# Kernel optimization log

Hardware: AMD Instinct MI355X
Metric: run time of the kernel (lower is better)

## Reference

```python
import jax, jax.numpy as jnp
import numpy as np

B, K, N = 8192, 10, 100
LAM = 1.0


def _vec_transpose_P():
    # 9x9 vec-transpose permutation: P[3i+j, 3j+i] = 1 (the _getP matrix)
    P = np.zeros((9, 9), dtype=np.float32)
    for i in range(3):
        for j in range(3):
            P[3 * i + j, 3 * j + i] = 1.0
    return jnp.asarray(P)


def setup_inputs() -> dict:
    key = jax.random.key(0)
    k1, k2, k3 = jax.random.split(key, 3)
    weights = jax.random.uniform(k1, (N, 1), dtype=jnp.float32) + 0.1  # positive weights
    model_keypoints = jax.random.normal(k2, (K, 3, N), dtype=jnp.float32)
    y = jax.random.normal(k3, (B, 3, N), dtype=jnp.float32)
    return {"y": y, "weights": weights, "model_keypoints": model_keypoints}


def _pace_forward(y, weights, model_keypoints):
    n = model_keypoints.shape[-1]
    k = model_keypoints.shape[0]
    bsz = y.shape[0]
    w = weights                                  # (N,1)
    wsum = w.sum()
    b = model_keypoints                          # (K,3,N)
    b_w = (b @ w) / wsum                         # (K,3,1)
    sw = jnp.sqrt(w[:, 0])                       # (N,)

    # ---- precomputed constants (original __init__) ----
    bar_b = sw[None, None, :] * (b - b_w)                    # (K,3,N)
    bar_B = bar_b.transpose(0, 2, 1).reshape(k, 3 * n).T     # (3N,K), row idx 3n+a
    bar_H = 2.0 * (bar_B.T @ bar_B + LAM * jnp.eye(k, dtype=y.dtype))
    Hinv = jnp.linalg.inv(bar_H)
    Ht = Hinv @ jnp.ones((k, 1), dtype=y.dtype)
    denom = Ht.sum()
    G = Hinv - (Ht @ Ht.T) / denom               # (K,K)
    g = Ht / denom                               # (K,1)
    GBt = G @ bar_B.T                            # (K,3N)
    M = jnp.concatenate([2.0 * bar_B @ GBt - jnp.eye(3 * n, dtype=y.dtype),
                         2.0 * jnp.sqrt(LAM) * GBt], axis=0)       # (3N+K,3N)
    h = jnp.concatenate([bar_B @ g, jnp.sqrt(LAM) * g], axis=0)    # (3N+K,1)
    P = _vec_transpose_P().astype(y.dtype)

    # ---- forward ----
    y_w = (y @ w) / wsum                         # (B,3,1)
    bar_y = sw[None, None, :] * (y - y_w)        # (B,3,N)

    # E_b = M @ kron(Ybar_b^T, I3) @ P, done batched without materializing kron:
    # (M @ kron(Y^T, I3))[m, 3j+a] = sum_n M[m, 3n+a] * Y[j, n]
    Mr = M.reshape(-1, n, 3)                                  # Mr[m, nn, a] = M[m, 3nn+a]
    MB = jnp.einsum('mna,bjn->bmja', Mr, bar_y)               # (B,3N+K,3,3)
    E = MB.reshape(bsz, -1, 9) @ P                            # (B,3N+K,9)
    q00 = h[:, 0] @ h[:, 0]                                   # scalar h^T h
    hE = jnp.einsum('m,bmc->bc', h[:, 0], E)                  # (B,9)
    Q11 = jnp.einsum('bmc,bmd->bcd', E, E)                    # (B,9,9)
    top = jnp.concatenate([jnp.broadcast_to(q00, (bsz, 1, 1)), hE[:, None, :]], axis=2)
    bot = jnp.concatenate([hE[:, :, None], Q11], axis=2)
    Q = jnp.concatenate([top, bot], axis=1)                   # (B,10,10)

    # SDP relaxation: at a tight optimum X = v v^T with v the minimizer of v^T Q v,
    # recovered here as the eigenvector of Q with smallest eigenvalue (batched eigh)
    _, evec = jnp.linalg.eigh(Q)
    v = evec[:, :, 0]                                         # (B,10), ascending order
    v = v / v[:, :1]                                          # homogenize: v[0] = 1
    R = v[:, 1:].reshape(bsz, 3, 3).transpose(0, 2, 1)        # (B,3,3)

    # shape coefficients: c = 2 * G B^T * kron(I_N, R^T) vec(bar_y) + g
    RTy = jnp.einsum('bra,brn->bna', R, bar_y).reshape(bsz, 3 * n)   # idx 3n+a
    c = 2.0 * jnp.einsum('km,bm->bk', GBt, RTy)[:, :, None] + g[None, :, :]  # (B,K,1)
    # translation: t = y_w - R b_w^T c
    t = y_w - R @ jnp.einsum('ka,bko->bao', b_w[:, :, 0], c)  # (B,3,1)
    return R, t, c


def reference(y, weights, model_keypoints):
    return _pace_forward(y, weights, model_keypoints)
```

## Files before the change

kernel.cpp:

```cpp
#include <hip/hip_runtime.h>
#include <math.h>

#define SM_WSUM 0
#define SM_RWS  1
#define SM_Q00  2
#define SM_Z2   4
#define SM_BS   16
#define SM_W    48
#define SM_G    148
#define SM_GV   248
#define SM_BW   260
#define SM_SIZE 292

__host__ __device__ constexpr int TRI(int p, int q) { return p*10 - (p*(p+1))/2 + q; }
__host__ __device__ constexpr int SIDX(int a, int b) { return (a<=b) ? TRI(a,b) : TRI(b,a); }

__global__ __launch_bounds__(64, 1) void pace_fused(const float* __restrict__ y,
                                                    const float* __restrict__ w,
                                                    const float* __restrict__ mk,
                                                    float* __restrict__ out) {
  __shared__ __attribute__((aligned(16))) float sc[3200];
  __shared__ float sm[SM_SIZE];
  __shared__ __attribute__((aligned(16))) float scr[5760];
  const int tid = threadIdx.x;
  const int b = blockIdx.x*64 + tid;
  const float* yb = y + b*300;

  float4 c0 = *(const float4*)(yb);
  float4 c1 = *(const float4*)(yb+100);
  float4 c2 = *(const float4*)(yb+200);

  float yw[3];

  {
    float* s_mb = scr;
    float* s_w  = scr+3000;
    float* s_sw = scr+3104;
    float* s_bw = scr+3208;
    float* s_C  = scr+3240;
    float* s_Hi = scr+3340;
    float* s_G  = scr+3440;
    float* s_T  = scr+3540;
    float* s_gv = scr+3640;
    float* s_Ht = scr+3656;
    float* s_z  = scr+3672;

    for (int i=tid;i<3000;i+=64) s_mb[i]=mk[i];
    for (int i=tid;i<100;i+=64){ float x=w[i]; s_w[i]=x; s_sw[i]=sqrtf(x); }
    __syncthreads();

    float a = s_w[tid] + ((tid<36)? s_w[tid+64] : 0.f);
    #pragma unroll
    for (int m=32;m;m>>=1) a += __shfl_xor(a,m);
    const float wsum = a;
    const float rws = 1.0f/a;

    if (tid<30){
      const float4* p=(const float4*)&s_mb[tid*100];
      const float4* q=(const float4*)&s_w[0];
      float acc=0;
      #pragma unroll 5
      for (int j=0;j<25;j++){ float4 x=p[j], yv=q[j];
        acc=fmaf(x.x,yv.x,acc); acc=fmaf(x.y,yv.y,acc);
        acc=fmaf(x.z,yv.z,acc); acc=fmaf(x.w,yv.w,acc); }
      s_bw[tid]=acc*rws;
    }
    __syncthreads();
    for (int i=tid;i<3000;i+=64){ int r=i/100, n=i-r*100; s_mb[i]=s_sw[n]*(s_mb[i]-s_bw[r]); }
    __syncthreads();
    for (int e=tid;e<100;e+=64){
      int k=e/10, k2=e-10*k;
      const float4* p1=(const float4*)&s_mb[k*300];
      const float4* p2=(const float4*)&s_mb[k2*300];
      float acc=0;
      #pragma unroll 5
      for (int j=0;j<75;j++){ float4 x=p1[j], yv=p2[j];
        acc=fmaf(x.x,yv.x,acc); acc=fmaf(x.y,yv.y,acc);
        acc=fmaf(x.z,yv.z,acc); acc=fmaf(x.w,yv.w,acc); }
      s_C[e]=acc;
    }
    __syncthreads();
    float R[20];
    {
      int row=(tid<10)? tid : 0;
      #pragma unroll
      for (int c=0;c<10;c++) R[c]=2.0f*(s_C[row*10+c]+(c==row?1.0f:0.0f));
      #pragma unroll
      for (int c=0;c<10;c++) R[10+c]=(c==row)?1.0f:0.0f;
    }
    #pragma unroll
    for (int p=0;p<10;p++){
      float appv=__shfl(R[p],p);
      float ra=1.0f/appv;
      float fr=R[p];
      #pragma unroll
      for (int c=0;c<20;c++){
        float pc=__shfl(R[c],p)*ra;
        R[c]=(tid==p)? pc : fmaf(-fr,pc,R[c]);
      }
    }
    float ht=0.f;
    if (tid<10){
      #pragma unroll
      for (int c=0;c<10;c++){ s_Hi[tid*10+c]=R[10+c]; ht+=R[10+c]; }
      s_Ht[tid]=ht;
    }
    float hv=(tid<10)? ht : 0.f;
    #pragma unroll
    for (int m=32;m;m>>=1) hv+=__shfl_xor(hv,m);
    const float rden=1.0f/hv;
    if (tid<10) s_gv[tid]=ht*rden;
    __syncthreads();
    for (int e=tid;e<100;e+=64){ int r=e/10,c=e-10*r; s_G[e]=s_Hi[e]-s_Ht[r]*s_Ht[c]*rden; }
    __syncthreads();
    for (int e=tid;e<100;e+=64){
      int r=e/10,c=e-10*r; float acc=0;
      #pragma unroll
      for (int j=0;j<10;j++) acc+=(s_C[r*10+j]+(r==j?1.0f:0.0f))*s_G[j*10+c];
      s_T[e]=acc;
    }
    __syncthreads();
    for (int e=tid;e<100;e+=64){
      int r=e/10,c=e-10*r; float acc=0;
      #pragma unroll
      for (int j=0;j<10;j++) acc+=s_G[r*10+j]*s_T[j*10+c];
      sm[SM_W+e]=4.0f*acc-4.0f*s_G[e];
      sm[SM_G+e]=s_G[e];
    }
    if (tid<10){
      float acc=0;
      #pragma unroll
      for (int j=0;j<10;j++) acc+=(s_C[tid*10+j]+(tid==j?1.0f:0.0f))*s_gv[j];
      s_z[tid]=acc;
    }
    __syncthreads();
    if (tid<10){
      float acc=0;
      #pragma unroll
      for (int j=0;j<10;j++) acc+=s_G[tid*10+j]*s_z[j];
      sm[SM_Z2+tid]=2.0f*acc-s_gv[tid];
    }
    float qv=0.f;
    if (tid<10){
      float acc=0;
      #pragma unroll
      for (int c=0;c<10;c++) acc+=s_C[tid*10+c]*s_gv[c];
      qv=s_gv[tid]*acc+s_gv[tid]*s_gv[tid];
    }
    #pragma unroll
    for (int m=32;m;m>>=1) qv+=__shfl_xor(qv,m);
    if (tid==0){ sm[SM_WSUM]=wsum; sm[SM_RWS]=rws; sm[SM_Q00]=qv; sm[3]=0.f; }
    for (int i=tid;i<3200;i+=64){
      int n=i>>5, e=i&31; float v;
      if (e==0) v=s_w[n];
      else if (e==31) v=0.f;
      else v=s_mb[(e-1)*100+n]*s_sw[n];
      sc[i]=v;
    }
    if (tid<30){
      const float4* p=(const float4*)&s_mb[tid*100];
      const float4* q=(const float4*)&s_sw[0];
      float acc=0;
      #pragma unroll 5
      for (int j=0;j<25;j++){ float4 x=p[j], yv=q[j];
        acc=fmaf(x.x,yv.x,acc); acc=fmaf(x.y,yv.y,acc);
        acc=fmaf(x.z,yv.z,acc); acc=fmaf(x.w,yv.w,acc); }
      sm[SM_BS+tid]=acc;
    }
    if (tid<10) sm[SM_GV+tid]=s_gv[tid];
    if (tid<30) sm[SM_BW+tid]=s_bw[tid];
    __syncthreads();
  }

  float* sF = scr;

  float swy0=0,swy1=0,swy2=0;
  float s00=0,s01=0,s02=0,s11=0,s12=0,s22=0;
  float F0[90];
  #pragma unroll
  for (int i=0;i<90;i++) F0[i]=0.f;

  #pragma unroll 1
  for (int g=0; g<25; ++g) {
    float4 n0, n1, n2;
    if (g<24) {
      n0 = *(const float4*)(yb+4*g+4);
      n1 = *(const float4*)(yb+104+4*g);
      n2 = *(const float4*)(yb+204+4*g);
    }
    float ax[4]={c0.x,c0.y,c0.z,c0.w};
    float bx[4]={c1.x,c1.y,c1.z,c1.w};
    float gx[4]={c2.x,c2.y,c2.z,c2.w};
    #pragma unroll
    for (int u=0;u<4;u++) {
      const int n = 4*g+u;
      float cf[32];
      const float4* cp = (const float4*)&sc[n*32];
      #pragma unroll
      for (int r=0;r<8;r++) ((float4*)cf)[r] = cp[r];
      float y0=ax[u], y1=bx[u], y2=gx[u];
      float wn=cf[0];
      float wy0=wn*y0, wy1=wn*y1, wy2=wn*y2;
      swy0+=wy0; swy1+=wy1; swy2+=wy2;
      s00+=wy0*y0; s01+=wy0*y1; s02+=wy0*y2; s11+=wy1*y1; s12+=wy1*y2; s22+=wy2*y2;
      #pragma unroll
      for (int k=0;k<10;k++) {
        #pragma unroll
        for (int j=0;j<3;j++) {
          float bcv=cf[1+k*3+j];
          F0[k*9+j*3+0]+=bcv*y0; F0[k*9+j*3+1]+=bcv*y1; F0[k*9+j*3+2]+=bcv*y2;
        }
      }
    }
    if (g<24) { c0=n0; c1=n1; c2=n2; }
  }

  const float wsum=sm[SM_WSUM], rws=sm[SM_RWS], q00=sm[SM_Q00];
  yw[0]=swy0*rws; yw[1]=swy1*rws; yw[2]=swy2*rws;
  float G3[9];
  G3[0]=s00-wsum*yw[0]*yw[0];
  G3[4]=s11-wsum*yw[1]*yw[1];
  G3[8]=s22-wsum*yw[2]*yw[2];
  G3[1]=G3[3]=s01-wsum*yw[0]*yw[1];
  G3[2]=G3[6]=s02-wsum*yw[0]*yw[2];
  G3[5]=G3[7]=s12-wsum*yw[1]*yw[2];
  #pragma unroll
  for (int k=0;k<10;k++)
    #pragma unroll
    for (int j=0;j<3;j++)
      #pragma unroll
      for (int i=0;i<3;i++)
        F0[k*9+j*3+i] -= yw[i]*sm[SM_BS+k*3+j];
  #pragma unroll
  for (int m=0;m<90;m++) sF[m*64+tid]=F0[m];
  float hE[9];
  #pragma unroll
  for (int m=0;m<9;m++) {
    float acc=0;
    #pragma unroll
    for (int k=0;k<10;k++) acc += sm[SM_Z2+k]*F0[k*9+m];
    hE[m]=acc;
  }

  float A[55];
  A[TRI(0,0)]=q00;
  #pragma unroll
  for (int m=0;m<9;m++) A[TRI(0,1+m)]=hE[m];
  #pragma unroll
  for (int mp=0;mp<9;mp++) {
    float t2[10];
    #pragma unroll
    for (int k=0;k<10;k++) {
      float acc=0;
      #pragma unroll
      for (int k2=0;k2<10;k2++) acc += sm[SM_W+k*10+k2]*F0[k2*9+mp];
      t2[k]=acc;
    }
    #pragma unroll
    for (int m=0;m<9;m++) {
      if (m>mp) continue;
      float acc = ((m/3)==(mp/3)) ? G3[(m%3)*3+(mp%3)] : 0.f;
      #pragma unroll
      for (int k=0;k<10;k++) acc += F0[k*9+m]*t2[k];
      A[TRI(1+m,1+mp)]=acc;
    }
  }

  constexpr int OFFK[8] = {0,9,17,24,30,35,39,42};
  float vhh[44], beta[8], ee[9];

  #pragma unroll
  for (int k=0;k<8;k++) {
    float nrm2 = 0.f;
    #pragma unroll
    for (int i=1;i<10;i++){ if (i<k+1) continue; float xi=A[SIDX(i,k)]; nrm2=fmaf(xi,xi,nrm2); }
    float x0 = A[SIDX(k+1,k)];
    float nr = sqrtf(nrm2);
    float alpha = -copysignf(nr, x0);
    bool ok = nrm2 > 1e-30f;
    float v1 = x0 - alpha;
    float vtv = -2.0f*alpha*v1;
    float bh = ok ? 2.0f*__builtin_amdgcn_rcpf(vtv) : 0.f;
    beta[k]=bh; ee[k]= ok ? alpha : x0;
    float vv[10];
    #pragma unroll
    for (int i=0;i<10;i++){
      if (i<k+1) { vv[i]=0.f; continue; }
      vv[i] = (i==k+1)? v1 : A[SIDX(i,k)];
    }
    #pragma unroll
    for (int i=0;i<9;i++){ if (i>=9-k) break; vhh[OFFK[k]+i]=vv[k+1+i]; }
    float p[10];
    #pragma unroll
    for (int i=0;i<10;i++){
      if (i<k+1){ p[i]=0.f; continue; }
      float acc=0;
      #pragma unroll
      for (int j=1;j<10;j++){ if (j<k+1) continue; acc += A[SIDX(i,j)]*vv[j]; }
      p[i]=bh*acc;
    }
    float Kc=0.f;
    #pragma unroll
    for (int i=1;i<10;i++){ if (i<k+1) continue; Kc = fmaf(vv[i],p[i],Kc); }
    Kc *= 0.5f*bh;
    float wv[10];
    #pragma unroll
    for (int i=0;i<10;i++){ wv[i] = p[i] - Kc*vv[i]; }
    #pragma unroll
    for (int i=1;i<10;i++){
      if (i<k+1) continue;
      #pragma unroll
      for (int j=1;j<10;j++){
        if (j<i) continue;
        A[TRI(i,j)] -= vv[i]*wv[j] + wv[i]*vv[j];
      }
    }
  }
  ee[8] = A[TRI(8,9)];
  float dd[10];
  #pragma unroll
  for (int i=0;i<10;i++) dd[i]=A[TRI(i,i)];
  float esq[9];
  #pragma unroll
  for (int i=0;i<9;i++) esq[i]=ee[i]*ee[i];

  float scaleT=0.f, lo=1e30f, hi=1e30f;
  #pragma unroll
  for (int i=0;i<10;i++){
    float r = ((i>0)?fabsf(ee[i-1]):0.f) + ((i<9)?fabsf(ee[i]):0.f);
    scaleT = fmaxf(scaleT, fabsf(dd[i])+r);
    lo = fminf(lo, dd[i]-r);
    hi = fminf(hi, dd[i]);
  }
  hi += 1e-6f*scaleT + 1e-30f;
  const float pm = 1e-12f*scaleT + 1e-37f;

  #pragma unroll 1
  for (int it=0; it<18; ++it){
    float mid = 0.5f*(lo+hi);
    float q = dd[0]-mid;
    q = (fabsf(q)<pm) ? ((q<0.f)?-pm:pm) : q;
    int cnt = (q<0.f);
    #pragma unroll
    for (int i=1;i<10;i++){
      q = dd[i]-mid - esq[i-1]*__builtin_amdgcn_rcpf(q);
      q = (fabsf(q)<pm) ? ((q<0.f)?-pm:pm) : q;
      cnt += (q<0.f);
    }
    bool any = cnt>0;
    hi = any? mid : hi;
    lo = any? lo : mid;
  }
  const float sigma = lo - 1e-5f*scaleT - 1e-30f;
  const float pmL = 1e-8f*scaleT + 1e-37f;

  float lfac[9], iq[10];
  {
    float q = fmaxf(dd[0]-sigma, pmL);
    iq[0]=__builtin_amdgcn_rcpf(q);
    #pragma unroll
    for (int i=1;i<10;i++){
      lfac[i-1] = ee[i-1]*iq[i-1];
      q = fmaxf(dd[i]-sigma - ee[i-1]*lfac[i-1], pmL);
      iq[i]=__builtin_amdgcn_rcpf(q);
    }
  }
  float xv[10];
  #pragma unroll
  for (int i=0;i<10;i++) xv[i]=1.f;
  #pragma unroll 1
  for (int itr=0; itr<3; ++itr){
    #pragma unroll
    for (int i=1;i<10;i++){ float v = xv[i] - lfac[i-1]*xv[i-1]; xv[i]=fminf(fmaxf(v,-1e15f),1e15f); }
    #pragma unroll
    for (int i=0;i<10;i++){ float v = xv[i]*iq[i]; xv[i]=fminf(fmaxf(v,-1e15f),1e15f); }
    #pragma unroll
    for (int i=8;i>=0;i--){ float v = xv[i] - lfac[i]*xv[i+1]; xv[i]=fminf(fmaxf(v,-1e15f),1e15f); }
    float nn=0.f;
    #pragma unroll
    for (int i=0;i<10;i++) nn = fmaf(xv[i],xv[i],nn);
    nn = fmaxf(nn, 1e-30f);
    float sc2 = rsqrtf(nn);
    #pragma unroll
    for (int i=0;i<10;i++) xv[i]*=sc2;
  }
  #pragma unroll
  for (int k=7;k>=0;k--){
    float s=0.f;
    #pragma unroll
    for (int i=0;i<9;i++){ if (i>=9-k) break; s = fmaf(vhh[OFFK[k]+i], xv[k+1+i], s); }
    s *= beta[k];
    #pragma unroll
    for (int i=0;i<9;i++){ if (i>=9-k) break; xv[k+1+i] -= s*vhh[OFFK[k]+i]; }
  }

  float r0 = 1.0f/xv[0];
  float vn[10];
  vn[0]=1.f;
  #pragma unroll
  for (int m=1;m<10;m++) vn[m]=xv[m]*r0;

  #pragma unroll
  for (int i=0;i<3;i++)
    #pragma unroll
    for (int j=0;j<3;j++)
      out[b*9 + i*3 + j] = vn[1+3*j+i];

  float d[10];
  #pragma unroll
  for (int k=0;k<10;k++) {
    float acc=0;
    #pragma unroll
    for (int m=0;m<9;m++) acc += vn[1+m]*sF[(k*9+m)*64+tid];
    d[k]=acc;
  }
  float cv[10];
  #pragma unroll
  for (int k=0;k<10;k++) {
    float acc=0;
    #pragma unroll
    for (int k2=0;k2<10;k2++) acc += sm[SM_G+k*10+k2]*d[k2];
    cv[k]=2.0f*acc + sm[SM_GV+k];
  }
  float e0=0,e1=0,e2v=0;
  #pragma unroll
  for (int k=0;k<10;k++) {
    e0 += sm[SM_BW+k*3+0]*cv[k];
    e1 += sm[SM_BW+k*3+1]*cv[k];
    e2v += sm[SM_BW+k*3+2]*cv[k];
  }
  #pragma unroll
  for (int i=0;i<3;i++) {
    float tv = yw[i] - (vn[1+0+i]*e0 + vn[1+3+i]*e1 + vn[1+6+i]*e2v);
    out[8192*9 + b*3 + i] = tv;
  }
  #pragma unroll
  for (int k=0;k<10;k++)
    out[8192*12 + b*10 + k] = cv[k];
}

extern "C" void kernel_launch(void* const* d_in, const int* in_sizes, int n_in,
                              void* d_out, int out_size, void* d_ws, size_t ws_size,
                              hipStream_t stream) {
  const float* y  = (const float*)d_in[0];
  const float* w  = (const float*)d_in[1];
  const float* mk = (const float*)d_in[2];
  float* out = (float*)d_out;
  pace_fused<<<128, 64, 0, stream>>>(y, w, mk, out);
}
```

Before: 120.3 us.

## Split each batch item across 8 lanes with DPP reductions and parallel bisection

Each batch item is now handled by 8 cooperating lanes instead of one, which raises the grid from 128 to 1024 blocks. The lanes split the N-loop accumulation and combine partial sums with DPP reductions, build Q columns in parallel through shared memory, and run a 9-way multisection eigenvalue search using ballot. The inverse iteration now works on a Cholesky factor of the shifted original Q, so the Householder back-transformation is dropped. The aim is to fill far more of the GPU than 128 single-wave blocks could. The cost is redundant per-block setup (the K×K inverse and constants are recomputed in all 1024 blocks), extra syncthreads, and fewer bisection steps, which may change precision.

```diff
diff --git a/kernel.cpp b/kernel.cpp
--- a/kernel.cpp
+++ b/kernel.cpp
@@ -12,25 +12,34 @@
 #define SM_BW   260
 #define SM_SIZE 292
 
-__host__ __device__ constexpr int TRI(int p, int q) { return p*10 - (p*(p+1))/2 + q; }
-__host__ __device__ constexpr int SIDX(int a, int b) { return (a<=b) ? TRI(a,b) : TRI(b,a); }
-
-__global__ __launch_bounds__(64, 1) void pace_fused(const float* __restrict__ y,
-                                                    const float* __restrict__ w,
-                                                    const float* __restrict__ mk,
-                                                    float* __restrict__ out) {
-  __shared__ __attribute__((aligned(16))) float sc[3200];
+__host__ __device__ constexpr int TRI(int p,int q){ return p*10-(p*(p+1))/2+q; }
+__host__ __device__ constexpr int SIDX(int a,int b){ return (a<=b)?TRI(a,b):TRI(b,a); }
+__host__ __device__ constexpr int LTRI(int i,int j){ return i*(i+1)/2+j; }
+
+template<int CTRL>
+__device__ __forceinline__ float dpp_add(float v){
+  int s = __builtin_amdgcn_mov_dpp(__float_as_int(v), CTRL, 0xF, 0xF, true);
+  return v + __int_as_float(s);
+}
+__device__ __forceinline__ float gsum8(float v){
+  v = dpp_add<0xB1>(v);
+  v = dpp_add<0x4E>(v);
+  v = dpp_add<0x141>(v);
+  return v;
+}
+
+__global__ __launch_bounds__(64,1) void pace_fused(const float* __restrict__ y,
+                                                   const float* __restrict__ w,
+                                                   const float* __restrict__ mk,
+                                                   float* __restrict__ out){
+  __shared__ __attribute__((aligned(16))) float sc[3600];
   __shared__ float sm[SM_SIZE];
-  __shared__ __attribute__((aligned(16))) float scr[5760];
-  const int tid = threadIdx.x;
-  const int b = blockIdx.x*64 + tid;
-  const float* yb = y + b*300;
-
-  float4 c0 = *(const float4*)(yb);
-  float4 c1 = *(const float4*)(yb+100);
-  float4 c2 = *(const float4*)(yb+200);
-
-  float yw[3];
+  __shared__ __attribute__((aligned(16))) float scr[3712];
+  const int tid  = threadIdx.x;
+  const int sub  = tid & 7;
+  const int item = tid >> 3;
+  const int gb   = blockIdx.x*8 + item;
+  const float* yb = y + gb*300;
 
   {
     float* s_mb = scr;
@@ -150,10 +159,10 @@
     #pragma unroll
     for (int m=32;m;m>>=1) qv+=__shfl_xor(qv,m);
     if (tid==0){ sm[SM_WSUM]=wsum; sm[SM_RWS]=rws; sm[SM_Q00]=qv; sm[3]=0.f; }
-    for (int i=tid;i<3200;i+=64){
-      int n=i>>5, e=i&31; float v;
+    for (int i=tid;i<3600;i+=64){
+      int n=i/36, e=i-36*n; float v;
       if (e==0) v=s_w[n];
-      else if (e==31) v=0.f;
+      else if (e>=31) v=0.f;
       else v=s_mb[(e-1)*100+n]*s_sw[n];
       sc[i]=v;
     }
@@ -172,152 +181,179 @@
     __syncthreads();
   }
 
-  float* sF = scr;
-
-  float swy0=0,swy1=0,swy2=0;
-  float s00=0,s01=0,s02=0,s11=0,s12=0,s22=0;
+  float* sF  = scr;
+  float* sD  = scr+736;
+  float* sQl = scr+832;
+  float* sG3 = scr+1280;
+
   float F0[90];
   #pragma unroll
   for (int i=0;i<90;i++) F0[i]=0.f;
-
-  #pragma unroll 1
-  for (int g=0; g<25; ++g) {
-    float4 n0, n1, n2;
-    if (g<24) {
-      n0 = *(const float4*)(yb+4*g+4);
-      n1 = *(const float4*)(yb+104+4*g);
-      n2 = *(const float4*)(yb+204+4*g);
-    }
-    float ax[4]={c0.x,c0.y,c0.z,c0.w};
-    float bx[4]={c1.x,c1.y,c1.z,c1.w};
-    float gx[4]={c2.x,c2.y,c2.z,c2.w};
-    #pragma unroll
-    for (int u=0;u<4;u++) {
-      const int n = 4*g+u;
-      float cf[32];
-      const float4* cp = (const float4*)&sc[n*32];
-      #pragma unroll
-      for (int r=0;r<8;r++) ((float4*)cf)[r] = cp[r];
-      float y0=ax[u], y1=bx[u], y2=gx[u];
-      float wn=cf[0];
-      float wy0=wn*y0, wy1=wn*y1, wy2=wn*y2;
-      swy0+=wy0; swy1+=wy1; swy2+=wy2;
-      s00+=wy0*y0; s01+=wy0*y1; s02+=wy0*y2; s11+=wy1*y1; s12+=wy1*y2; s22+=wy2*y2;
-      #pragma unroll
-      for (int k=0;k<10;k++) {
+  float swy0=0,swy1=0,swy2=0,s00=0,s01=0,s02=0,s11=0,s12=0,s22=0;
+
+  #pragma unroll
+  for (int mrep=0;mrep<4;++mrep){
+    int g=sub+8*mrep;
+    if (g<25){
+      float4 a4=*(const float4*)(yb+4*g);
+      float4 b4=*(const float4*)(yb+100+4*g);
+      float4 g4=*(const float4*)(yb+200+4*g);
+      float ax[4]={a4.x,a4.y,a4.z,a4.w};
+      float bx[4]={b4.x,b4.y,b4.z,b4.w};
+      float gx[4]={g4.x,g4.y,g4.z,g4.w};
+      #pragma unroll
+      for (int u=0;u<4;u++){
+        const float* cf=&sc[(4*g+u)*36];
+        float c[32];
         #pragma unroll
-        for (int j=0;j<3;j++) {
-          float bcv=cf[1+k*3+j];
-          F0[k*9+j*3+0]+=bcv*y0; F0[k*9+j*3+1]+=bcv*y1; F0[k*9+j*3+2]+=bcv*y2;
+        for (int r=0;r<8;r++) ((float4*)c)[r]=((const float4*)cf)[r];
+        float y0=ax[u],y1=bx[u],y2=gx[u];
+        float wn=c[0];
+        float wy0=wn*y0,wy1=wn*y1,wy2=wn*y2;
+        swy0+=wy0;swy1+=wy1;swy2+=wy2;
+        s00+=wy0*y0;s01+=wy0*y1;s02+=wy0*y2;s11+=wy1*y1;s12+=wy1*y2;s22+=wy2*y2;
+        #pragma unroll
+        for (int k=0;k<10;k++){
+          #pragma unroll
+          for (int j=0;j<3;j++){
+            float bcv=c[1+k*3+j];
+            F0[k*9+j*3+0]+=bcv*y0;
+            F0[k*9+j*3+1]+=bcv*y1;
+            F0[k*9+j*3+2]+=bcv*y2;
+          }
         }
       }
     }
-    if (g<24) { c0=n0; c1=n1; c2=n2; }
-  }
-
-  const float wsum=sm[SM_WSUM], rws=sm[SM_RWS], q00=sm[SM_Q00];
-  yw[0]=swy0*rws; yw[1]=swy1*rws; yw[2]=swy2*rws;
-  float G3[9];
-  G3[0]=s00-wsum*yw[0]*yw[0];
-  G3[4]=s11-wsum*yw[1]*yw[1];
-  G3[8]=s22-wsum*yw[2]*yw[2];
-  G3[1]=G3[3]=s01-wsum*yw[0]*yw[1];
-  G3[2]=G3[6]=s02-wsum*yw[0]*yw[2];
-  G3[5]=G3[7]=s12-wsum*yw[1]*yw[2];
-  #pragma unroll
-  for (int k=0;k<10;k++)
-    #pragma unroll
-    for (int j=0;j<3;j++)
-      #pragma unroll
-      for (int i=0;i<3;i++)
-        F0[k*9+j*3+i] -= yw[i]*sm[SM_BS+k*3+j];
-  #pragma unroll
-  for (int m=0;m<90;m++) sF[m*64+tid]=F0[m];
-  float hE[9];
-  #pragma unroll
-  for (int m=0;m<9;m++) {
-    float acc=0;
-    #pragma unroll
-    for (int k=0;k<10;k++) acc += sm[SM_Z2+k]*F0[k*9+m];
-    hE[m]=acc;
-  }
+  }
+  #pragma unroll
+  for (int e=0;e<90;e++) F0[e]=gsum8(F0[e]);
+  swy0=gsum8(swy0); swy1=gsum8(swy1); swy2=gsum8(swy2);
+  s00=gsum8(s00); s01=gsum8(s01); s02=gsum8(s02);
+  s11=gsum8(s11); s12=gsum8(s12); s22=gsum8(s22);
+
+  const float wsum=sm[SM_WSUM], rws=sm[SM_RWS];
+  const float yw0=swy0*rws, yw1=swy1*rws, yw2=swy2*rws;
+  float G3r[9];
+  G3r[0]=s00-wsum*yw0*yw0; G3r[4]=s11-wsum*yw1*yw1; G3r[8]=s22-wsum*yw2*yw2;
+  G3r[1]=G3r[3]=s01-wsum*yw0*yw1;
+  G3r[2]=G3r[6]=s02-wsum*yw0*yw2;
+  G3r[5]=G3r[7]=s12-wsum*yw1*yw2;
+  #pragma unroll
+  for (int k=0;k<10;k++){
+    float bs0=sm[SM_BS+k*3+0],bs1=sm[SM_BS+k*3+1],bs2=sm[SM_BS+k*3+2];
+    F0[k*9+0]-=yw0*bs0; F0[k*9+1]-=yw1*bs0; F0[k*9+2]-=yw2*bs0;
+    F0[k*9+3]-=yw0*bs1; F0[k*9+4]-=yw1*bs1; F0[k*9+5]-=yw2*bs1;
+    F0[k*9+6]-=yw0*bs2; F0[k*9+7]-=yw1*bs2; F0[k*9+8]-=yw2*bs2;
+  }
+  if (sub==0){
+    #pragma unroll
+    for (int e=0;e<90;e++) sF[item*90+e]=F0[e];
+    #pragma unroll
+    for (int e=0;e<9;e++) sG3[item*9+e]=G3r[e];
+  }
+  __syncthreads();
+
+  {
+    int mp=sub;
+    float fcol[10], t2[10];
+    #pragma unroll
+    for (int k=0;k<10;k++) fcol[k]=sF[item*90+k*9+mp];
+    #pragma unroll
+    for (int k=0;k<10;k++){
+      float acc=0;
+      #pragma unroll
+      for (int k2=0;k2<10;k2++) acc+=sm[SM_W+k*10+k2]*fcol[k2];
+      t2[k]=acc;
+    }
+    float he=0;
+    #pragma unroll
+    for (int k=0;k<10;k++) he+=sm[SM_Z2+k]*fcol[k];
+    sQl[item*56 + 1+mp]=he;
+    #pragma unroll 1
+    for (int m=0;m<=mp;m++){
+      float gd=sG3[item*9+(m%3)*3+(mp%3)];
+      float acc=((m/3)==(mp/3))? gd : 0.f;
+      #pragma unroll
+      for (int k=0;k<10;k++) acc+=sF[item*90+k*9+m]*t2[k];
+      int p=1+m, q=1+mp;
+      sQl[item*56 + p*10-((p*(p+1))>>1)+q]=acc;
+    }
+    if (sub==0){
+      mp=8;
+      #pragma unroll
+      for (int k=0;k<10;k++) fcol[k]=sF[item*90+k*9+mp];
+      #pragma unroll
+      for (int k=0;k<10;k++){
+        float acc=0;
+        #pragma unroll
+        for (int k2=0;k2<10;k2++) acc+=sm[SM_W+k*10+k2]*fcol[k2];
+        t2[k]=acc;
+      }
+      he=0;
+      #pragma unroll
+      for (int k=0;k<10;k++) he+=sm[SM_Z2+k]*fcol[k];
+      sQl[item*56 + 9]=he;
+      #pragma unroll 1
+      for (int m=0;m<=8;m++){
+        float gd=sG3[item*9+(m%3)*3+2];
+        float acc=((m/3)==2)? gd : 0.f;
+        #pragma unroll
+        for (int k=0;k<10;k++) acc+=sF[item*90+k*9+m]*t2[k];
+        int p=1+m, q=9;
+        sQl[item*56 + p*10-((p*(p+1))>>1)+q]=acc;
+      }
+      sQl[item*56 + 0]=sm[SM_Q00];
+    }
+  }
+  __syncthreads();
 
   float A[55];
-  A[TRI(0,0)]=q00;
-  #pragma unroll
-  for (int m=0;m<9;m++) A[TRI(0,1+m)]=hE[m];
-  #pragma unroll
-  for (int mp=0;mp<9;mp++) {
-    float t2[10];
-    #pragma unroll
-    for (int k=0;k<10;k++) {
-      float acc=0;
-      #pragma unroll
-      for (int k2=0;k2<10;k2++) acc += sm[SM_W+k*10+k2]*F0[k2*9+mp];
-      t2[k]=acc;
-    }
-    #pragma unroll
-    for (int m=0;m<9;m++) {
-      if (m>mp) continue;
-      float acc = ((m/3)==(mp/3)) ? G3[(m%3)*3+(mp%3)] : 0.f;
-      #pragma unroll
-      for (int k=0;k<10;k++) acc += F0[k*9+m]*t2[k];
-      A[TRI(1+m,1+mp)]=acc;
-    }
-  }
-
-  constexpr int OFFK[8] = {0,9,17,24,30,35,39,42};
-  float vhh[44], beta[8], ee[9];
-
-  #pragma unroll
-  for (int k=0;k<8;k++) {
-    float nrm2 = 0.f;
+  #pragma unroll
+  for (int e=0;e<55;e++) A[e]=sQl[item*56+e];
+  float dd[10], ee[9];
+  #pragma unroll
+  for (int k=0;k<8;k++){
+    float nrm2=0.f;
     #pragma unroll
     for (int i=1;i<10;i++){ if (i<k+1) continue; float xi=A[SIDX(i,k)]; nrm2=fmaf(xi,xi,nrm2); }
-    float x0 = A[SIDX(k+1,k)];
-    float nr = sqrtf(nrm2);
-    float alpha = -copysignf(nr, x0);
-    bool ok = nrm2 > 1e-30f;
-    float v1 = x0 - alpha;
-    float vtv = -2.0f*alpha*v1;
-    float bh = ok ? 2.0f*__builtin_amdgcn_rcpf(vtv) : 0.f;
-    beta[k]=bh; ee[k]= ok ? alpha : x0;
+    float x0=A[SIDX(k+1,k)];
+    float nr=sqrtf(nrm2);
+    float alpha=-copysignf(nr,x0);
+    bool ok=nrm2>1e-30f;
+    float v1=x0-alpha;
+    float vtv=-2.0f*alpha*v1;
+    float bh=ok?2.0f*__builtin_amdgcn_rcpf(vtv):0.f;
+    ee[k]=ok?alpha:x0;
     float vv[10];
     #pragma unroll
-    for (int i=0;i<10;i++){
-      if (i<k+1) { vv[i]=0.f; continue; }
-      vv[i] = (i==k+1)? v1 : A[SIDX(i,k)];
-    }
-    #pragma unroll
-    for (int i=0;i<9;i++){ if (i>=9-k) break; vhh[OFFK[k]+i]=vv[k+1+i]; }
+    for (int i=0;i<10;i++) vv[i]=(i<k+1)?0.f:((i==k+1)?v1:A[SIDX(i,k)]);
     float p[10];
     #pragma unroll
     for (int i=0;i<10;i++){
       if (i<k+1){ p[i]=0.f; continue; }
       float acc=0;
       #pragma unroll
-      for (int j=1;j<10;j++){ if (j<k+1) continue; acc += A[SIDX(i,j)]*vv[j]; }
+      for (int j=1;j<10;j++){ if (j<k+1) continue; acc+=A[SIDX(i,j)]*vv[j]; }
       p[i]=bh*acc;
     }
     float Kc=0.f;
     #pragma unroll
-    for (int i=1;i<10;i++){ if (i<k+1) continue; Kc = fmaf(vv[i],p[i],Kc); }
-    Kc *= 0.5f*bh;
+    for (int i=1;i<10;i++){ if (i<k+1) continue; Kc=fmaf(vv[i],p[i],Kc); }
+    Kc*=0.5f*bh;
     float wv[10];
     #pragma unroll
-    for (int i=0;i<10;i++){ wv[i] = p[i] - Kc*vv[i]; }
+    for (int i=0;i<10;i++) wv[i]=p[i]-Kc*vv[i];
     #pragma unroll
     for (int i=1;i<10;i++){
       if (i<k+1) continue;
       #pragma unroll
       for (int j=1;j<10;j++){
         if (j<i) continue;
-        A[TRI(i,j)] -= vv[i]*wv[j] + wv[i]*vv[j];
+        A[TRI(i,j)]-=vv[i]*wv[j]+wv[i]*vv[j];
       }
     }
   }
-  ee[8] = A[TRI(8,9)];
-  float dd[10];
+  ee[8]=A[TRI(8,9)];
   #pragma unroll
   for (int i=0;i<10;i++) dd[i]=A[TRI(i,i)];
   float esq[9];
@@ -327,116 +363,145 @@
   float scaleT=0.f, lo=1e30f, hi=1e30f;
   #pragma unroll
   for (int i=0;i<10;i++){
-    float r = ((i>0)?fabsf(ee[i-1]):0.f) + ((i<9)?fabsf(ee[i]):0.f);
-    scaleT = fmaxf(scaleT, fabsf(dd[i])+r);
-    lo = fminf(lo, dd[i]-r);
-    hi = fminf(hi, dd[i]);
-  }
-  hi += 1e-6f*scaleT + 1e-30f;
-  const float pm = 1e-12f*scaleT + 1e-37f;
-
+    float r=((i>0)?fabsf(ee[i-1]):0.f)+((i<9)?fabsf(ee[i]):0.f);
+    scaleT=fmaxf(scaleT,fabsf(dd[i])+r);
+    lo=fminf(lo,dd[i]-r);
+    hi=fminf(hi,dd[i]);
+  }
+  hi+=1e-6f*scaleT+1e-30f;
+  const float pm=1e-12f*scaleT+1e-37f;
+  const float r9=1.0f/9.0f;
   #pragma unroll 1
-  for (int it=0; it<18; ++it){
-    float mid = 0.5f*(lo+hi);
-    float q = dd[0]-mid;
-    q = (fabsf(q)<pm) ? ((q<0.f)?-pm:pm) : q;
-    int cnt = (q<0.f);
+  for (int it=0;it<6;++it){
+    float delta=(hi-lo)*r9;
+    float mid=lo+delta*(float)(sub+1);
+    float q=dd[0]-mid;
+    q=(fabsf(q)<pm)?((q<0.f)?-pm:pm):q;
+    int cnt=(q<0.f);
     #pragma unroll
     for (int i=1;i<10;i++){
-      q = dd[i]-mid - esq[i-1]*__builtin_amdgcn_rcpf(q);
-      q = (fabsf(q)<pm) ? ((q<0.f)?-pm:pm) : q;
-      cnt += (q<0.f);
-    }
-    bool any = cnt>0;
-    hi = any? mid : hi;
-    lo = any? lo : mid;
-  }
-  const float sigma = lo - 1e-5f*scaleT - 1e-30f;
-  const float pmL = 1e-8f*scaleT + 1e-37f;
-
-  float lfac[9], iq[10];
-  {
-    float q = fmaxf(dd[0]-sigma, pmL);
-    iq[0]=__builtin_amdgcn_rcpf(q);
-    #pragma unroll
-    for (int i=1;i<10;i++){
-      lfac[i-1] = ee[i-1]*iq[i-1];
-      q = fmaxf(dd[i]-sigma - ee[i-1]*lfac[i-1], pmL);
-      iq[i]=__builtin_amdgcn_rcpf(q);
+      q=dd[i]-mid-esq[i-1]*__builtin_amdgcn_rcpf(q);
+      q=(fabsf(q)<pm)?((q<0.f)?-pm:pm):q;
+      cnt+=(q<0.f);
+    }
+    unsigned long long bal=__ballot(cnt>0);
+    unsigned gb8=(unsigned)((bal>>(item*8))&0xFFull);
+    int js=gb8?(__ffs((int)gb8)-1):8;
+    float nhi=(js<8)?(lo+delta*(float)(js+1)):hi;
+    lo=lo+delta*(float)js;
+    hi=nhi;
+  }
+  const float sigma=lo-1e-5f*scaleT-1e-30f;
+  const float pmL=1e-8f*scaleT+1e-37f;
+
+  float Lc[55], rd[10];
+  #pragma unroll
+  for (int i=0;i<10;i++){
+    #pragma unroll
+    for (int j=0;j<10;j++){
+      if (j>i) continue;
+      float a=sQl[item*56+SIDX(j,i)]-((i==j)?sigma:0.f);
+      #pragma unroll
+      for (int t2=0;t2<9;t2++){
+        if (t2>=j) continue;
+        a-=Lc[LTRI(i,t2)]*Lc[LTRI(j,t2)];
+      }
+      if (j<i) Lc[LTRI(i,j)]=a*rd[j];
+      else { a=fmaxf(a,pmL); rd[i]=rsqrtf(a); Lc[LTRI(i,i)]=a*rd[i]; }
     }
   }
   float xv[10];
   #pragma unroll
   for (int i=0;i<10;i++) xv[i]=1.f;
   #pragma unroll 1
-  for (int itr=0; itr<3; ++itr){
-    #pragma unroll
-    for (int i=1;i<10;i++){ float v = xv[i] - lfac[i-1]*xv[i-1]; xv[i]=fminf(fmaxf(v,-1e15f),1e15f); }
-    #pragma unroll
-    for (int i=0;i<10;i++){ float v = xv[i]*iq[i]; xv[i]=fminf(fmaxf(v,-1e15f),1e15f); }
-    #pragma unroll
-    for (int i=8;i>=0;i--){ float v = xv[i] - lfac[i]*xv[i+1]; xv[i]=fminf(fmaxf(v,-1e15f),1e15f); }
+  for (int itr=0;itr<3;++itr){
+    #pragma unroll
+    for (int i=0;i<10;i++){
+      float acc=xv[i];
+      #pragma unroll
+      for (int j=0;j<9;j++){ if (j>=i) continue; acc-=Lc[LTRI(i,j)]*xv[j]; }
+      acc*=rd[i];
+      xv[i]=fminf(fmaxf(acc,-1e15f),1e15f);
+    }
+    #pragma unroll
+    for (int i=9;i>=0;i--){
+      float acc=xv[i];
+      #pragma unroll
+      for (int j=9;j>0;j--){ if (j<=i) continue; acc-=Lc[LTRI(j,i)]*xv[j]; }
+      acc*=rd[i];
+      xv[i]=fminf(fmaxf(acc,-1e15f),1e15f);
+    }
     float nn=0.f;
     #pragma unroll
-    for (int i=0;i<10;i++) nn = fmaf(xv[i],xv[i],nn);
-    nn = fmaxf(nn, 1e-30f);
-    float sc2 = rsqrtf(nn);
+    for (int i=0;i<10;i++) nn=fmaf(xv[i],xv[i],nn);
+    nn=fmaxf(nn,1e-30f);
+    float sc2=rsqrtf(nn);
     #pragma unroll
     for (int i=0;i<10;i++) xv[i]*=sc2;
   }
-  #pragma unroll
-  for (int k=7;k>=0;k--){
-    float s=0.f;
-    #pragma unroll
-    for (int i=0;i<9;i++){ if (i>=9-k) break; s = fmaf(vhh[OFFK[k]+i], xv[k+1+i], s); }
-    s *= beta[k];
-    #pragma unroll
-    for (int i=0;i<9;i++){ if (i>=9-k) break; xv[k+1+i] -= s*vhh[OFFK[k]+i]; }
-  }
-
-  float r0 = 1.0f/xv[0];
+  float r0=1.0f/xv[0];
   float vn[10];
   vn[0]=1.f;
   #pragma unroll
   for (int m=1;m<10;m++) vn[m]=xv[m]*r0;
 
-  #pragma unroll
-  for (int i=0;i<3;i++)
-    #pragma unroll
-    for (int j=0;j<3;j++)
-      out[b*9 + i*3 + j] = vn[1+3*j+i];
-
-  float d[10];
-  #pragma unroll
-  for (int k=0;k<10;k++) {
+  {
+    float dv=0;
+    #pragma unroll
+    for (int m=0;m<9;m++) dv+=vn[1+m]*sF[item*90+sub*9+m];
+    sD[item*10+sub]=dv;
+    if (sub<2){
+      float dv2=0;
+      #pragma unroll
+      for (int m=0;m<9;m++) dv2+=vn[1+m]*sF[item*90+(8+sub)*9+m];
+      sD[item*10+8+sub]=dv2;
+    }
+  }
+  __syncthreads();
+  float dreg[10];
+  #pragma unroll
+  for (int k=0;k<10;k++) dreg[k]=sD[item*10+k];
+  __syncthreads();
+  {
     float acc=0;
     #pragma unroll
-    for (int m=0;m<9;m++) acc += vn[1+m]*sF[(k*9+m)*64+tid];
-    d[k]=acc;
-  }
-  float cv[10];
-  #pragma unroll
-  for (int k=0;k<10;k++) {
-    float acc=0;
-    #pragma unroll
-    for (int k2=0;k2<10;k2++) acc += sm[SM_G+k*10+k2]*d[k2];
-    cv[k]=2.0f*acc + sm[SM_GV+k];
-  }
-  float e0=0,e1=0,e2v=0;
-  #pragma unroll
-  for (int k=0;k<10;k++) {
-    e0 += sm[SM_BW+k*3+0]*cv[k];
-    e1 += sm[SM_BW+k*3+1]*cv[k];
-    e2v += sm[SM_BW+k*3+2]*cv[k];
-  }
-  #pragma unroll
-  for (int i=0;i<3;i++) {
-    float tv = yw[i] - (vn[1+0+i]*e0 + vn[1+3+i]*e1 + vn[1+6+i]*e2v);
-    out[8192*9 + b*3 + i] = tv;
-  }
-  #pragma unroll
-  for (int k=0;k<10;k++)
-    out[8192*12 + b*10 + k] = cv[k];
+    for (int k2=0;k2<10;k2++) acc+=sm[SM_G+sub*10+k2]*dreg[k2];
+    float cvk=2.0f*acc+sm[SM_GV+sub];
+    out[98304+gb*10+sub]=cvk;
+    sD[item*10+sub]=cvk;
+    if (sub<2){
+      int kk=8+sub;
+      float acc2=0;
+      #pragma unroll
+      for (int k2=0;k2<10;k2++) acc2+=sm[SM_G+kk*10+k2]*dreg[k2];
+      float cvk2=2.0f*acc2+sm[SM_GV+kk];
+      out[98304+gb*10+kk]=cvk2;
+      sD[item*10+kk]=cvk2;
+    }
+  }
+  __syncthreads();
+  float cvr[10];
+  #pragma unroll
+  for (int k=0;k<10;k++) cvr[k]=sD[item*10+k];
+  float e0=0,e1=0,e2=0;
+  #pragma unroll
+  for (int k=0;k<10;k++){
+    e0+=sm[SM_BW+k*3+0]*cvr[k];
+    e1+=sm[SM_BW+k*3+1]*cvr[k];
+    e2+=sm[SM_BW+k*3+2]*cvr[k];
+  }
+  if (sub==2){
+    #pragma unroll
+    for (int i=0;i<3;i++)
+      #pragma unroll
+      for (int j=0;j<3;j++)
+        out[gb*9+i*3+j]=vn[1+3*j+i];
+  }
+  if (sub==3){
+    out[73728+gb*3+0]=yw0-(vn[1]*e0+vn[4]*e1+vn[7]*e2);
+    out[73728+gb*3+1]=yw1-(vn[2]*e0+vn[5]*e1+vn[8]*e2);
+    out[73728+gb*3+2]=yw2-(vn[3]*e0+vn[6]*e1+vn[9]*e2);
+  }
 }
 
 extern "C" void kernel_launch(void* const* d_in, const int* in_sizes, int n_in,
@@ -446,5 +511,5 @@
   const float* w  = (const float*)d_in[1];
   const float* mk = (const float*)d_in[2];
   float* out = (float*)d_out;
-  pace_fused<<<128, 64, 0, stream>>>(y, w, mk, out);
+  pace_fused<<<1024, 64, 0, stream>>>(y, w, mk, out);
 }
```

After: 104.6 us. 13.1% less time.
